# Kernel tuning notes

Measured on AMD Instinct MI355X. Metric: run time of the kernel, lower is better.

Reference implementation:

```python
import jax, jax.numpy as jnp
import numpy as np

N_SRC = 50000
N_DST = 50000
E = 800000
IN_DIM = 128
OUT_DIM = 128
H = 8
DK = OUT_DIM // H  # 16
SLOPE = 0.2  # leaky relu negative slope


def setup_inputs() -> dict:
    key = jax.random.key(0)
    ks = jax.random.split(key, 12)
    std_lin = 0.05  # stand-in for xavier_normal scale
    inp = {
        "feat_src": jax.random.normal(ks[0], (N_SRC, IN_DIM), jnp.float32),
        "feat_dst": jax.random.normal(ks[1], (N_DST, IN_DIM), jnp.float32),
        "src_idx": jax.random.randint(ks[2], (E,), 0, N_SRC, jnp.int32),
        "dst_idx": jnp.sort(jax.random.randint(ks[3], (E,), 0, N_DST, jnp.int32)),
        "Wq": jax.random.normal(ks[4], (OUT_DIM, IN_DIM), jnp.float32) * std_lin,
        "bq": jnp.zeros((OUT_DIM,), jnp.float32),
        "Wk": jax.random.normal(ks[5], (OUT_DIM, IN_DIM), jnp.float32) * std_lin,
        "bk": jnp.zeros((OUT_DIM,), jnp.float32),
        "Wv": jax.random.normal(ks[6], (OUT_DIM, IN_DIM), jnp.float32) * std_lin,
        "bv": jnp.zeros((OUT_DIM,), jnp.float32),
        "relation_att": jax.random.normal(ks[7], (H, DK, DK), jnp.float32) * 0.2,
        "Wo": jax.random.normal(ks[8], (OUT_DIM, OUT_DIM), jnp.float32) * std_lin,
        "bo": jnp.zeros((OUT_DIM,), jnp.float32),
    }
    return inp


def reference(feat_src, feat_dst, src_idx, dst_idx,
              Wq, bq, Wk, bk, Wv, bv, relation_att, Wo, bo):
    n_dst = feat_dst.shape[0]
    # node-level projections, split into heads
    q = (feat_dst @ Wq.T + bq).reshape(-1, H, DK)   # (N_dst, H, DK)
    k = (feat_src @ Wk.T + bk).reshape(-1, H, DK)   # (N_src, H, DK)
    v = (feat_src @ Wv.T + bv).reshape(-1, H, DK)   # (N_src, H, DK)
    # relation-aware transform of keys (per head)
    k = jnp.einsum('nhd,hde->nhe', k, relation_att)  # (N_src, H, DK)
    scale = jnp.sqrt(jnp.asarray(DK, feat_src.dtype))
    # per-edge, per-head attention logits
    logits = jnp.einsum('ehd,ehd->eh', q[dst_idx], k[src_idx]) / scale  # (E, H)
    logits = jnp.where(logits >= 0, logits, SLOPE * logits)             # leaky relu
    # numerically stable edge softmax over incoming edges of each dst
    seg_max = jax.ops.segment_max(logits, dst_idx, num_segments=n_dst)
    seg_max = jnp.where(jnp.isfinite(seg_max), seg_max, 0.0)
    ex = jnp.exp(logits - seg_max[dst_idx])
    denom = jax.ops.segment_sum(ex, dst_idx, num_segments=n_dst)
    a = ex / denom[dst_idx]                                             # (E, H)
    # weighted message aggregation: sum_e v[src_e] * a_e
    msg = v[src_idx] * a[:, :, None]                                    # (E, H, DK)
    h = jax.ops.segment_sum(msg, dst_idx, num_segments=n_dst)           # (N_dst, H, DK)
    out = h.reshape(n_dst, OUT_DIM) @ Wo.T + bo
    return out
```

## Files before the change

### kernel.cpp

```cpp
#include <hip/hip_runtime.h>
#include <math.h>

#define DIM 128
#define H 8
#define DK 16
#define BM 64
#define LDB 136
#define SSTAGE 128

typedef __attribute__((ext_vector_type(8))) short short8;
typedef __attribute__((ext_vector_type(4))) float f32x4;
typedef unsigned short u16;
typedef unsigned int u32;

__device__ inline u16 f2bf(float f) {
    union { float f; u32 u; } v; v.f = f;
    u32 r = v.u + 0x7fffu + ((v.u >> 16) & 1u);
    return (u16)(r >> 16);
}
__device__ inline float bfl(u32 u) { union { u32 u; float f; } v; v.u = u << 16; return v.f; }
__device__ inline float bfh(u32 u) { union { u32 u; float f; } v; v.u = u & 0xffff0000u; return v.f; }

__global__ __launch_bounds__(256, 4)
void proj_qkv(const float* __restrict__ fsrc, const float* __restrict__ fdst,
              const float* __restrict__ Wq, const float* __restrict__ bq,
              const float* __restrict__ Wk2, const float* __restrict__ bk2,
              const float* __restrict__ Wv, const float* __restrict__ bv,
              u16* __restrict__ qo, u16* __restrict__ ko, u16* __restrict__ vo,
              int n_dst, int n_src, int gq, int gs) {
    __shared__ __align__(16) u16 wl[DIM * LDB];
    const int bid = blockIdx.x;
    const float *X, *W, *B; u16* Y; int n, tile;
    if (bid < gq)           { X = fdst; W = Wq;  B = bq;  Y = qo; n = n_dst; tile = bid; }
    else if (bid < gq + gs) { X = fsrc; W = Wk2; B = bk2; Y = ko; n = n_src; tile = bid - gq; }
    else                    { X = fsrc; W = Wv;  B = bv;  Y = vo; n = n_src; tile = bid - gq - gs; }

    const int tid = threadIdx.x;
#pragma unroll
    for (int it = 0; it < 8; ++it) {
        int c8 = it * 256 + tid;
        int row = c8 >> 4, ck = c8 & 15;
        const float4* s = (const float4*)&W[(size_t)row * DIM + ck * 8];
        float4 f0 = s[0], f1 = s[1];
        short8 u;
        u[0] = (short)f2bf(f0.x); u[1] = (short)f2bf(f0.y);
        u[2] = (short)f2bf(f0.z); u[3] = (short)f2bf(f0.w);
        u[4] = (short)f2bf(f1.x); u[5] = (short)f2bf(f1.y);
        u[6] = (short)f2bf(f1.z); u[7] = (short)f2bf(f1.w);
        *(short8*)&wl[row * LDB + ck * 8] = u;
    }
    __syncthreads();
    const int lane = tid & 63, wave = tid >> 6;
    const int lrow = lane & 15, kg = lane >> 4;
    const int rbase = tile * BM + wave * 16;
    int xr = rbase + lrow; if (xr > n - 1) xr = n - 1;
    const float* xp = X + (size_t)xr * DIM + kg * 8;

    f32x4 acc[8];
#pragma unroll
    for (int j = 0; j < 8; ++j) acc[j] = (f32x4){0.f, 0.f, 0.f, 0.f};

#pragma unroll
    for (int kc = 0; kc < 4; ++kc) {
        float4 a0 = *(const float4*)(xp + kc * 32);
        float4 a1 = *(const float4*)(xp + kc * 32 + 4);
        short8 af;
        af[0] = (short)f2bf(a0.x); af[1] = (short)f2bf(a0.y);
        af[2] = (short)f2bf(a0.z); af[3] = (short)f2bf(a0.w);
        af[4] = (short)f2bf(a1.x); af[5] = (short)f2bf(a1.y);
        af[6] = (short)f2bf(a1.z); af[7] = (short)f2bf(a1.w);
#pragma unroll
        for (int j = 0; j < 8; ++j) {
            short8 bf = *(const short8*)&wl[(j * 16 + lrow) * LDB + kc * 32 + kg * 8];
            acc[j] = __builtin_amdgcn_mfma_f32_16x16x32_bf16(af, bf, acc[j], 0, 0, 0);
        }
    }
#pragma unroll
    for (int r = 0; r < 4; ++r) {
        int gr = rbase + kg * 4 + r;
        if (gr < n) {
#pragma unroll
            for (int j = 0; j < 8; ++j) {
                int c = j * 16 + lrow;
                Y[(size_t)gr * DIM + c] = f2bf(acc[j][r] + B[c]);
            }
        }
    }
}

__global__ __launch_bounds__(256, 4)
void gemm_mfma_b(const u16* __restrict__ X, const float* __restrict__ W,
                 const float* __restrict__ b, float* __restrict__ Y, int n) {
    __shared__ __align__(16) u16 wl[DIM * LDB];
    const int tid = threadIdx.x;
#pragma unroll
    for (int it = 0; it < 8; ++it) {
        int c8 = it * 256 + tid;
        int row = c8 >> 4, ck = c8 & 15;
        const float4* s = (const float4*)&W[(size_t)row * DIM + ck * 8];
        float4 f0 = s[0], f1 = s[1];
        short8 u;
        u[0] = (short)f2bf(f0.x); u[1] = (short)f2bf(f0.y);
        u[2] = (short)f2bf(f0.z); u[3] = (short)f2bf(f0.w);
        u[4] = (short)f2bf(f1.x); u[5] = (short)f2bf(f1.y);
        u[6] = (short)f2bf(f1.z); u[7] = (short)f2bf(f1.w);
        *(short8*)&wl[row * LDB + ck * 8] = u;
    }
    __syncthreads();
    const int lane = tid & 63, wave = tid >> 6;
    const int lrow = lane & 15, kg = lane >> 4;
    const int rbase = blockIdx.x * BM + wave * 16;
    int xr = rbase + lrow; if (xr > n - 1) xr = n - 1;
    const u16* xp = X + (size_t)xr * DIM + kg * 8;

    f32x4 acc[8];
#pragma unroll
    for (int j = 0; j < 8; ++j) acc[j] = (f32x4){0.f, 0.f, 0.f, 0.f};

#pragma unroll
    for (int kc = 0; kc < 4; ++kc) {
        short8 af = *(const short8*)(xp + kc * 32);
#pragma unroll
        for (int j = 0; j < 8; ++j) {
            short8 bf = *(const short8*)&wl[(j * 16 + lrow) * LDB + kc * 32 + kg * 8];
            acc[j] = __builtin_amdgcn_mfma_f32_16x16x32_bf16(af, bf, acc[j], 0, 0, 0);
        }
    }
#pragma unroll
    for (int r = 0; r < 4; ++r) {
        int gr = rbase + kg * 4 + r;
        if (gr < n) {
#pragma unroll
            for (int j = 0; j < 8; ++j) {
                int c = j * 16 + lrow;
                Y[(size_t)gr * DIM + c] = acc[j][r] + b[c];
            }
        }
    }
}

__global__ void fold_relation(const float* __restrict__ Wk, const float* __restrict__ bk,
                              const float* __restrict__ R, float* __restrict__ Wk2,
                              float* __restrict__ bk2) {
    const int o = blockIdx.x;
    const int t = threadIdx.x;
    const int h = o >> 4, e = o & 15;
    float acc = 0.f;
#pragma unroll
    for (int d = 0; d < DK; ++d)
        acc = fmaf(R[h * 256 + d * 16 + e], Wk[(size_t)(h * 16 + d) * DIM + t], acc);
    Wk2[(size_t)o * DIM + t] = acc;
    if (t == 0) {
        float bb = 0.f;
#pragma unroll
        for (int d = 0; d < DK; ++d) bb = fmaf(R[h * 256 + d * 16 + e], bk[h * 16 + d], bb);
        bk2[o] = bb;
    }
}

__global__ void seg_bounds(const int* __restrict__ didx, int* __restrict__ seg,
                           int E, int n_dst) {
    int e = blockIdx.x * blockDim.x + threadIdx.x;
    if (e >= E) return;
    int d = didx[e];
    int dp = (e == 0) ? -1 : didx[e - 1];
    for (int x = dp + 1; x <= d; ++x) seg[x] = e;
    if (e == E - 1)
        for (int x = d + 1; x <= n_dst; ++x) seg[x] = E;
}

__global__ void edge_attn5(const u16* __restrict__ q, const u16* __restrict__ k,
                           const u16* __restrict__ v, const int* __restrict__ sidx,
                           const int* __restrict__ seg, u16* __restrict__ hout) {
    const int dst = blockIdx.x;
    const int t = threadIdx.x;
    const int g = t >> 4, dg = t & 15;

    __shared__ int sidx_s[SSTAGE];
    __shared__ float red[16][9];

    const int s0 = seg[dst], s1 = seg[dst + 1];

    float qf[8];
    {
        uint4 qa = ((const uint4*)q)[(size_t)dst * 16 + dg];
        qf[0] = bfl(qa.x); qf[1] = bfh(qa.x); qf[2] = bfl(qa.y); qf[3] = bfh(qa.y);
        qf[4] = bfl(qa.z); qf[5] = bfh(qa.z); qf[6] = bfl(qa.w); qf[7] = bfh(qa.w);
    }

    const uint4* kp = (const uint4*)k;
    const uint4* vp = (const uint4*)v;

    float ssum = 0.f;
    float acc[8];
#pragma unroll
    for (int j = 0; j < 8; ++j) acc[j] = 0.f;

    for (int base = s0; base < s1; base += SSTAGE) {
        const int nst = min(SSTAGE, s1 - base);
        __syncthreads();
        if (t < nst) sidx_s[t] = sidx[base + t];
        __syncthreads();

#pragma unroll 2
        for (int c = 0; c < nst; c += 8) {
            const int e = c + g;
            const bool valid = e < nst;
            const int row = sidx_s[valid ? e : 0];
            uint4 k4 = kp[(size_t)row * 16 + dg];
            float d = 0.f;
            d = fmaf(bfl(k4.x), qf[0], d); d = fmaf(bfh(k4.x), qf[1], d);
            d = fmaf(bfl(k4.y), qf[2], d); d = fmaf(bfh(k4.y), qf[3], d);
            d = fmaf(bfl(k4.z), qf[4], d); d = fmaf(bfh(k4.z), qf[5], d);
            d = fmaf(bfl(k4.w), qf[6], d); d = fmaf(bfh(k4.w), qf[7], d);
            d += __shfl_xor(d, 1);
            float lg = d * 0.25f;
            lg = (lg >= 0.f) ? lg : 0.2f * lg;
            float p = valid ? __expf(lg) : 0.f;
            ssum += p;
            uint4 v4 = vp[(size_t)row * 16 + dg];
            acc[0] = fmaf(p, bfl(v4.x), acc[0]); acc[1] = fmaf(p, bfh(v4.x), acc[1]);
            acc[2] = fmaf(p, bfl(v4.y), acc[2]); acc[3] = fmaf(p, bfh(v4.y), acc[3]);
            acc[4] = fmaf(p, bfl(v4.z), acc[4]); acc[5] = fmaf(p, bfh(v4.z), acc[5]);
            acc[6] = fmaf(p, bfl(v4.w), acc[6]); acc[7] = fmaf(p, bfh(v4.w), acc[7]);
        }
    }

#pragma unroll
    for (int j = 0; j < 8; ++j) {
        acc[j] += __shfl_xor(acc[j], 16);
        acc[j] += __shfl_xor(acc[j], 32);
    }
    ssum += __shfl_xor(ssum, 16);
    ssum += __shfl_xor(ssum, 32);

    if (t >= 64 && t < 80) {
#pragma unroll
        for (int j = 0; j < 8; ++j) red[t - 64][j] = acc[j];
        red[t - 64][8] = ssum;
    }
    __syncthreads();
    if (t < 16) {
        float s = ssum + red[t][8];
        float inv = (s > 0.f) ? 1.f / s : 0.f;
        u16 o[8];
#pragma unroll
        for (int j = 0; j < 8; ++j) o[j] = f2bf((acc[j] + red[t][j]) * inv);
        uint4 pk;
        pk.x = (u32)o[0] | ((u32)o[1] << 16);
        pk.y = (u32)o[2] | ((u32)o[3] << 16);
        pk.z = (u32)o[4] | ((u32)o[5] << 16);
        pk.w = (u32)o[6] | ((u32)o[7] << 16);
        ((uint4*)hout)[(size_t)dst * 16 + t] = pk;
    }
}

extern "C" void kernel_launch(void* const* d_in, const int* in_sizes, int n_in,
                              void* d_out, int out_size, void* d_ws, size_t ws_size,
                              hipStream_t stream) {
    const float* feat_src = (const float*)d_in[0];
    const float* feat_dst = (const float*)d_in[1];
    const int*   src_idx  = (const int*)d_in[2];
    const int*   dst_idx  = (const int*)d_in[3];
    const float* Wq = (const float*)d_in[4];
    const float* bq = (const float*)d_in[5];
    const float* Wk = (const float*)d_in[6];
    const float* bk = (const float*)d_in[7];
    const float* Wv = (const float*)d_in[8];
    const float* bv = (const float*)d_in[9];
    const float* R  = (const float*)d_in[10];
    const float* Wo = (const float*)d_in[11];
    const float* bo = (const float*)d_in[12];

    const int n_src = in_sizes[0] / DIM;
    const int n_dst = in_sizes[1] / DIM;
    const int E     = in_sizes[2];

    float* out = (float*)d_out;
    u16* q   = (u16*)d_ws;
    u16* kk  = q  + (size_t)n_dst * DIM;
    u16* vv  = kk + (size_t)n_src * DIM;
    u16* hag = vv + (size_t)n_src * DIM;
    int* seg = (int*)(hag + (size_t)n_dst * DIM);
    size_t segEnd = ((size_t)(n_dst + 1) + 3) & ~(size_t)3;
    float* Wk2 = (float*)(seg + segEnd);
    float* bk2 = Wk2 + DIM * DIM;

    const int gq = (n_dst + BM - 1) / BM;
    const int gs = (n_src + BM - 1) / BM;

    seg_bounds<<<(E + 255) / 256, 256, 0, stream>>>(dst_idx, seg, E, n_dst);
    fold_relation<<<DIM, DIM, 0, stream>>>(Wk, bk, R, Wk2, bk2);
    proj_qkv<<<gq + 2 * gs, 256, 0, stream>>>(feat_src, feat_dst, Wq, bq, Wk2, bk2,
                                              Wv, bv, q, kk, vv, n_dst, n_src, gq, gs);
    edge_attn5<<<n_dst, DIM, 0, stream>>>(q, kk, vv, src_idx, seg, hag);
    gemm_mfma_b<<<gq, 256, 0, stream>>>(hag, Wo, bo, out, n_dst);
}
```

Measured before the change: 104.3 us.

## Interleave K and V rows and use one wave per destination with head-per-lane

```diff
diff --git a/kernel.cpp b/kernel.cpp
--- a/kernel.cpp
+++ b/kernel.cpp
@@ -6,7 +6,6 @@
 #define DK 16
 #define BM 64
 #define LDB 136
-#define SSTAGE 128
 
 typedef __attribute__((ext_vector_type(8))) short short8;
 typedef __attribute__((ext_vector_type(4))) float f32x4;
@@ -26,14 +25,14 @@
               const float* __restrict__ Wq, const float* __restrict__ bq,
               const float* __restrict__ Wk2, const float* __restrict__ bk2,
               const float* __restrict__ Wv, const float* __restrict__ bv,
-              u16* __restrict__ qo, u16* __restrict__ ko, u16* __restrict__ vo,
+              u16* __restrict__ qo, u16* __restrict__ kvo,
               int n_dst, int n_src, int gq, int gs) {
     __shared__ __align__(16) u16 wl[DIM * LDB];
     const int bid = blockIdx.x;
-    const float *X, *W, *B; u16* Y; int n, tile;
-    if (bid < gq)           { X = fdst; W = Wq;  B = bq;  Y = qo; n = n_dst; tile = bid; }
-    else if (bid < gq + gs) { X = fsrc; W = Wk2; B = bk2; Y = ko; n = n_src; tile = bid - gq; }
-    else                    { X = fsrc; W = Wv;  B = bv;  Y = vo; n = n_src; tile = bid - gq - gs; }
+    const float *X, *W, *B; u16* Y; int n, tile, ldy, coff;
+    if (bid < gq)           { X = fdst; W = Wq;  B = bq;  Y = qo;  n = n_dst; tile = bid;           ldy = 128; coff = 0; }
+    else if (bid < gq + gs) { X = fsrc; W = Wk2; B = bk2; Y = kvo; n = n_src; tile = bid - gq;      ldy = 256; coff = 0; }
+    else                    { X = fsrc; W = Wv;  B = bv;  Y = kvo; n = n_src; tile = bid - gq - gs; ldy = 256; coff = 128; }
 
     const int tid = threadIdx.x;
 #pragma unroll
@@ -82,7 +81,7 @@
 #pragma unroll
             for (int j = 0; j < 8; ++j) {
                 int c = j * 16 + lrow;
-                Y[(size_t)gr * DIM + c] = f2bf(acc[j][r] + B[c]);
+                Y[(size_t)gr * ldy + coff + c] = f2bf(acc[j][r] + B[c]);
             }
         }
     }
@@ -169,89 +168,87 @@
         for (int x = d + 1; x <= n_dst; ++x) seg[x] = E;
 }
 
-__global__ void edge_attn5(const u16* __restrict__ q, const u16* __restrict__ k,
-                           const u16* __restrict__ v, const int* __restrict__ sidx,
-                           const int* __restrict__ seg, u16* __restrict__ hout) {
+__global__ __launch_bounds__(64)
+void edge_attn6(const u16* __restrict__ q, const u16* __restrict__ kv,
+                const int* __restrict__ sidx, const int* __restrict__ seg,
+                u16* __restrict__ hout) {
     const int dst = blockIdx.x;
     const int t = threadIdx.x;
-    const int g = t >> 4, dg = t & 15;
-
-    __shared__ int sidx_s[SSTAGE];
-    __shared__ float red[16][9];
+    const int g = t >> 3, h = t & 7;
 
     const int s0 = seg[dst], s1 = seg[dst + 1];
 
-    float qf[8];
-    {
-        uint4 qa = ((const uint4*)q)[(size_t)dst * 16 + dg];
-        qf[0] = bfl(qa.x); qf[1] = bfh(qa.x); qf[2] = bfl(qa.y); qf[3] = bfh(qa.y);
-        qf[4] = bfl(qa.z); qf[5] = bfh(qa.z); qf[6] = bfl(qa.w); qf[7] = bfh(qa.w);
-    }
-
-    const uint4* kp = (const uint4*)k;
-    const uint4* vp = (const uint4*)v;
+    const uint4* qp = (const uint4*)q;
+    uint4 qa = qp[(size_t)dst * 16 + h * 2];
+    uint4 qb = qp[(size_t)dst * 16 + h * 2 + 1];
+    float qf[16];
+    qf[0]  = bfl(qa.x); qf[1]  = bfh(qa.x); qf[2]  = bfl(qa.y); qf[3]  = bfh(qa.y);
+    qf[4]  = bfl(qa.z); qf[5]  = bfh(qa.z); qf[6]  = bfl(qa.w); qf[7]  = bfh(qa.w);
+    qf[8]  = bfl(qb.x); qf[9]  = bfh(qb.x); qf[10] = bfl(qb.y); qf[11] = bfh(qb.y);
+    qf[12] = bfl(qb.z); qf[13] = bfh(qb.z); qf[14] = bfl(qb.w); qf[15] = bfh(qb.w);
+
+    const uint4* kvp = (const uint4*)kv;
 
     float ssum = 0.f;
-    float acc[8];
-#pragma unroll
-    for (int j = 0; j < 8; ++j) acc[j] = 0.f;
-
-    for (int base = s0; base < s1; base += SSTAGE) {
-        const int nst = min(SSTAGE, s1 - base);
-        __syncthreads();
-        if (t < nst) sidx_s[t] = sidx[base + t];
-        __syncthreads();
+    float acc[16];
+#pragma unroll
+    for (int j = 0; j < 16; ++j) acc[j] = 0.f;
 
 #pragma unroll 2
-        for (int c = 0; c < nst; c += 8) {
-            const int e = c + g;
-            const bool valid = e < nst;
-            const int row = sidx_s[valid ? e : 0];
-            uint4 k4 = kp[(size_t)row * 16 + dg];
-            float d = 0.f;
-            d = fmaf(bfl(k4.x), qf[0], d); d = fmaf(bfh(k4.x), qf[1], d);
-            d = fmaf(bfl(k4.y), qf[2], d); d = fmaf(bfh(k4.y), qf[3], d);
-            d = fmaf(bfl(k4.z), qf[4], d); d = fmaf(bfh(k4.z), qf[5], d);
-            d = fmaf(bfl(k4.w), qf[6], d); d = fmaf(bfh(k4.w), qf[7], d);
-            d += __shfl_xor(d, 1);
-            float lg = d * 0.25f;
-            lg = (lg >= 0.f) ? lg : 0.2f * lg;
-            float p = valid ? __expf(lg) : 0.f;
-            ssum += p;
-            uint4 v4 = vp[(size_t)row * 16 + dg];
-            acc[0] = fmaf(p, bfl(v4.x), acc[0]); acc[1] = fmaf(p, bfh(v4.x), acc[1]);
-            acc[2] = fmaf(p, bfl(v4.y), acc[2]); acc[3] = fmaf(p, bfh(v4.y), acc[3]);
-            acc[4] = fmaf(p, bfl(v4.z), acc[4]); acc[5] = fmaf(p, bfh(v4.z), acc[5]);
-            acc[6] = fmaf(p, bfl(v4.w), acc[6]); acc[7] = fmaf(p, bfh(v4.w), acc[7]);
-        }
-    }
-
-#pragma unroll
-    for (int j = 0; j < 8; ++j) {
+    for (int e = s0 + g; e < s1; e += 8) {
+        const int row = sidx[e];
+        const uint4* kb = kvp + (size_t)row * 32 + h * 2;
+        uint4 k0 = kb[0], k1 = kb[1];
+        uint4 v0 = kb[16], v1 = kb[17];
+        float d = 0.f;
+        d = fmaf(bfl(k0.x), qf[0], d);  d = fmaf(bfh(k0.x), qf[1], d);
+        d = fmaf(bfl(k0.y), qf[2], d);  d = fmaf(bfh(k0.y), qf[3], d);
+        d = fmaf(bfl(k0.z), qf[4], d);  d = fmaf(bfh(k0.z), qf[5], d);
+        d = fmaf(bfl(k0.w), qf[6], d);  d = fmaf(bfh(k0.w), qf[7], d);
+        d = fmaf(bfl(k1.x), qf[8], d);  d = fmaf(bfh(k1.x), qf[9], d);
+        d = fmaf(bfl(k1.y), qf[10], d); d = fmaf(bfh(k1.y), qf[11], d);
+        d = fmaf(bfl(k1.z), qf[12], d); d = fmaf(bfh(k1.z), qf[13], d);
+        d = fmaf(bfl(k1.w), qf[14], d); d = fmaf(bfh(k1.w), qf[15], d);
+        float lg = d * 0.25f;
+        lg = (lg >= 0.f) ? lg : 0.2f * lg;
+        const float p = __expf(lg);
+        ssum += p;
+        acc[0]  = fmaf(p, bfl(v0.x), acc[0]);  acc[1]  = fmaf(p, bfh(v0.x), acc[1]);
+        acc[2]  = fmaf(p, bfl(v0.y), acc[2]);  acc[3]  = fmaf(p, bfh(v0.y), acc[3]);
+        acc[4]  = fmaf(p, bfl(v0.z), acc[4]);  acc[5]  = fmaf(p, bfh(v0.z), acc[5]);
+        acc[6]  = fmaf(p, bfl(v0.w), acc[6]);  acc[7]  = fmaf(p, bfh(v0.w), acc[7]);
+        acc[8]  = fmaf(p, bfl(v1.x), acc[8]);  acc[9]  = fmaf(p, bfh(v1.x), acc[9]);
+        acc[10] = fmaf(p, bfl(v1.y), acc[10]); acc[11] = fmaf(p, bfh(v1.y), acc[11]);
+        acc[12] = fmaf(p, bfl(v1.z), acc[12]); acc[13] = fmaf(p, bfh(v1.z), acc[13]);
+        acc[14] = fmaf(p, bfl(v1.w), acc[14]); acc[15] = fmaf(p, bfh(v1.w), acc[15]);
+    }
+
+#pragma unroll
+    for (int j = 0; j < 16; ++j) {
+        acc[j] += __shfl_xor(acc[j], 8);
         acc[j] += __shfl_xor(acc[j], 16);
         acc[j] += __shfl_xor(acc[j], 32);
     }
+    ssum += __shfl_xor(ssum, 8);
     ssum += __shfl_xor(ssum, 16);
     ssum += __shfl_xor(ssum, 32);
 
-    if (t >= 64 && t < 80) {
-#pragma unroll
-        for (int j = 0; j < 8; ++j) red[t - 64][j] = acc[j];
-        red[t - 64][8] = ssum;
-    }
-    __syncthreads();
-    if (t < 16) {
-        float s = ssum + red[t][8];
-        float inv = (s > 0.f) ? 1.f / s : 0.f;
-        u16 o[8];
-#pragma unroll
-        for (int j = 0; j < 8; ++j) o[j] = f2bf((acc[j] + red[t][j]) * inv);
-        uint4 pk;
-        pk.x = (u32)o[0] | ((u32)o[1] << 16);
-        pk.y = (u32)o[2] | ((u32)o[3] << 16);
-        pk.z = (u32)o[4] | ((u32)o[5] << 16);
-        pk.w = (u32)o[6] | ((u32)o[7] << 16);
-        ((uint4*)hout)[(size_t)dst * 16 + t] = pk;
+    if (g == 0) {
+        const float inv = (ssum > 0.f) ? 1.f / ssum : 0.f;
+        u16 o[16];
+#pragma unroll
+        for (int j = 0; j < 16; ++j) o[j] = f2bf(acc[j] * inv);
+        uint4 pa, pb;
+        pa.x = (u32)o[0]  | ((u32)o[1]  << 16);
+        pa.y = (u32)o[2]  | ((u32)o[3]  << 16);
+        pa.z = (u32)o[4]  | ((u32)o[5]  << 16);
+        pa.w = (u32)o[6]  | ((u32)o[7]  << 16);
+        pb.x = (u32)o[8]  | ((u32)o[9]  << 16);
+        pb.y = (u32)o[10] | ((u32)o[11] << 16);
+        pb.z = (u32)o[12] | ((u32)o[13] << 16);
+        pb.w = (u32)o[14] | ((u32)o[15] << 16);
+        ((uint4*)hout)[(size_t)dst * 16 + h * 2]     = pa;
+        ((uint4*)hout)[(size_t)dst * 16 + h * 2 + 1] = pb;
     }
 }
 
@@ -278,9 +275,8 @@
 
     float* out = (float*)d_out;
     u16* q   = (u16*)d_ws;
-    u16* kk  = q  + (size_t)n_dst * DIM;
-    u16* vv  = kk + (size_t)n_src * DIM;
-    u16* hag = vv + (size_t)n_src * DIM;
+    u16* kv  = q  + (size_t)n_dst * DIM;
+    u16* hag = kv + (size_t)n_src * 2 * DIM;
     int* seg = (int*)(hag + (size_t)n_dst * DIM);
     size_t segEnd = ((size_t)(n_dst + 1) + 3) & ~(size_t)3;
     float* Wk2 = (float*)(seg + segEnd);
@@ -292,7 +288,7 @@
     seg_bounds<<<(E + 255) / 256, 256, 0, stream>>>(dst_idx, seg, E, n_dst);
     fold_relation<<<DIM, DIM, 0, stream>>>(Wk, bk, R, Wk2, bk2);
     proj_qkv<<<gq + 2 * gs, 256, 0, stream>>>(feat_src, feat_dst, Wq, bq, Wk2, bk2,
-                                              Wv, bv, q, kk, vv, n_dst, n_src, gq, gs);
-    edge_attn5<<<n_dst, DIM, 0, stream>>>(q, kk, vv, src_idx, seg, hag);
+                                              Wv, bv, q, kv, n_dst, n_src, gq, gs);
+    edge_attn6<<<n_dst, 64, 0, stream>>>(q, kv, src_idx, seg, hag);
     gemm_mfma_b<<<gq, 256, 0, stream>>>(hag, Wo, bo, out, n_dst);
 }
```

After: 104.9 us. No clear change (+0.6%).
